# Performance work log

Hardware: AMD Instinct MI355X
Metric: run time of the kernel (lower is better)

## Reference

```python
import jax, jax.numpy as jnp
import numpy as np

N, M, D = 4, 512, 1024
H = 16
DK = D // H


def setup_inputs() -> dict:
    rng = jax.random.key(0)
    ks = jax.random.split(rng, 11)
    w = lambda k: jax.random.normal(k, (D, D), jnp.float32) * 0.02
    b = lambda k: jax.random.normal(k, (D,), jnp.float32) * 0.02
    return {
        "query": jax.random.normal(ks[0], (N, M, D), jnp.float32),
        "key": jax.random.normal(ks[1], (N, M, D), jnp.float32),
        "value": jax.random.normal(ks[2], (N, M, D), jnp.float32),
        "Wq": w(ks[3]), "bq": b(ks[4]),
        "Wk": w(ks[5]), "bk": b(ks[6]),
        "Wv": w(ks[7]), "bv": b(ks[8]),
        "Wo": w(ks[9]), "bo": b(ks[10]),
    }


def reference(query, key, value, Wq, bq, Wk, bk, Wv, bv, Wo, bo):
    n, m, d = query.shape
    h, dk = H, d // H
    # torch Linear: y = x @ W.T + b
    q = (query @ Wq.T + bq).reshape(n, m, h, dk)
    k = (key @ Wk.T + bk).reshape(n, m, h, dk)
    v = (value @ Wv.T + bv).reshape(n, m, h, dk)
    # per-token channel outer product: [n,m,h,dk,dk]
    scores = jnp.einsum('nmhd,nmhq->nmhdq', q, k) / np.float32(np.sqrt(dk))
    p_attn = jax.nn.softmax(scores, axis=-1)
    # contract score block with value channels: [n,m,h,dk]
    ctx = jnp.einsum('nmhdq,nmhq->nmhd', p_attn, v).reshape(n, m, d)
    return ctx @ Wo.T + bo
```

## Files before the change

### kernel.cpp

```cpp
#include <hip/hip_runtime.h>
#include <hip/hip_bf16.h>
#include <stdint.h>
#include <stddef.h>

typedef __bf16 bf16_t;
typedef __attribute__((ext_vector_type(8))) __bf16 bf16x8;
typedef __attribute__((ext_vector_type(4))) float f32x4;
typedef __attribute__((ext_vector_type(2))) float f32x2;

#define TOK 2048
#define DMODEL 1024
#define NHEAD 16

__device__ __forceinline__ void gload_lds16(const void* g, void* l) {
  __builtin_amdgcn_global_load_lds(
      (const __attribute__((address_space(1))) void*)g,
      (__attribute__((address_space(3))) void*)l, 16, 0, 0);
}

struct CvtArgs {
  const float* src[7];
  bf16_t* dst[7];
  int n[7];
};

__global__ __launch_bounds__(256) void cvt_kernel(CvtArgs a) {
  const int arr = blockIdx.y;
  const int n = a.n[arr];
  const int i = blockIdx.x;
  int base;
  if (arr < 3) {
    const int xcd = i & 7, s = i >> 3;
    base = xcd * (256 * DMODEL) + s * 2048;
  } else {
    base = i * 2048;
  }
  const int e = base + threadIdx.x * 8;
  if (e >= n) return;
  const float* s = a.src[arr];
  bf16_t* d = a.dst[arr];
  f32x4 x0 = *(const f32x4*)(s + e);
  f32x4 x1 = *(const f32x4*)(s + e + 4);
  bf16x8 o;
  o[0] = (bf16_t)x0[0]; o[1] = (bf16_t)x0[1]; o[2] = (bf16_t)x0[2]; o[3] = (bf16_t)x0[3];
  o[4] = (bf16_t)x1[0]; o[5] = (bf16_t)x1[1]; o[6] = (bf16_t)x1[2]; o[7] = (bf16_t)x1[3];
  *(bf16x8*)(d + e) = o;
}

struct GArgs {
  const bf16_t* A[3];
  const bf16_t* W[3];
  const float* bias[3];
  void* C[3];
};

template <bool QKV3, int MI, int NJ, int OCC, typename CT>
__global__ __launch_bounds__(256, OCC) void gemmS(GArgs g) {
  constexpr int K = DMODEL, N = DMODEL;
  constexpr int nt = K / 64;
  constexpr int AR = 32 * MI;
  constexpr int BR = 32 * NJ;

  const int i = blockIdx.x;
  const int xcd = i & 7, slot = i >> 3;
  int z, bm, bn;
  if (QKV3) {
    z = slot >> 5;
    const int s = slot & 31;
    bm = (xcd * 2 + (s >> 4)) * AR;
    bn = (s & 15) * BR;
  } else {
    z = 0;
    bm = (xcd * 4 + (slot >> 5)) * AR;
    bn = (slot & 31) * BR;
  }

  const bf16_t* __restrict__ A = g.A[z];
  const bf16_t* __restrict__ W = g.W[z];
  const float* __restrict__ bias = g.bias[z];
  CT* __restrict__ C = (CT*)g.C[z];

  __shared__ alignas(16) bf16_t As[2][AR * 64];
  __shared__ alignas(16) bf16_t Bs[2][BR * 64];

  const int tid = threadIdx.x;
  const int wv = tid >> 6, lane = tid & 63;
  const int wr = (wv >> 1) * (16 * MI);
  const int wc = (wv & 1) * (16 * NJ);
  const int lm = lane & 15, lch = lane >> 4;
  const int cr4 = (lane >> 4) * 4;

  const int sr8 = lane >> 3;
  const int sc = (lane & 7) ^ sr8;
  const bf16_t* Asrc = A + (size_t)(bm + wv * 8 * MI + sr8) * K + sc * 8;
  const bf16_t* Wsrc = W + (size_t)(bn + wv * 8 * NJ + sr8) * K + sc * 8;

  f32x4 acc[MI][NJ] = {};

#define STAGE(T)                                                               \
  {                                                                            \
    const int _b = (T) & 1;                                                    \
    _Pragma("unroll") for (int j = 0; j < MI; ++j)                             \
        gload_lds16(Asrc + (size_t)(j * 8) * K + (T) * 64,                     \
                    &As[_b][(wv * 8 * MI + j * 8) * 64]);                      \
    _Pragma("unroll") for (int j = 0; j < NJ; ++j)                             \
        gload_lds16(Wsrc + (size_t)(j * 8) * K + (T) * 64,                     \
                    &Bs[_b][(wv * 8 * NJ + j * 8) * 64]);                      \
  }

  STAGE(0);

#pragma unroll 1
  for (int T = 0; T < nt; ++T) {
    __syncthreads();
    if (T + 1 < nt) STAGE(T + 1);
    __builtin_amdgcn_sched_barrier(0);

    const int b = T & 1;
#pragma unroll
    for (int kk = 0; kk < 2; ++kk) {
      bf16x8 fa[MI], fb[NJ];
#pragma unroll
      for (int ii = 0; ii < MI; ++ii) {
        const int ra = wr + ii * 16 + lm;
        fa[ii] = *(const bf16x8*)&As[b][ra * 64 + (((kk * 4 + lch) ^ (ra & 7)) * 8)];
      }
#pragma unroll
      for (int jj = 0; jj < NJ; ++jj) {
        const int rb = wc + jj * 16 + lm;
        fb[jj] = *(const bf16x8*)&Bs[b][rb * 64 + (((kk * 4 + lch) ^ (rb & 7)) * 8)];
      }
#pragma unroll
      for (int ii = 0; ii < MI; ++ii)
#pragma unroll
        for (int jj = 0; jj < NJ; ++jj)
          acc[ii][jj] = __builtin_amdgcn_mfma_f32_16x16x32_bf16(
              fa[ii], fb[jj], acc[ii][jj], 0, 0, 0);
    }
  }
#undef STAGE

#pragma unroll
  for (int ii = 0; ii < MI; ++ii)
#pragma unroll
    for (int jj = 0; jj < NJ; ++jj) {
      const int col = bn + wc + jj * 16 + lm;
      const float bvv = bias[col];
#pragma unroll
      for (int r = 0; r < 4; ++r) {
        const int row = bm + wr + ii * 16 + cr4 + r;
        C[(size_t)row * N + col] = (CT)(acc[ii][jj][r] + bvv);
      }
    }
}

__global__ __launch_bounds__(256) void attn_kernel(
    const bf16_t* __restrict__ q, const bf16_t* __restrict__ k,
    const bf16_t* __restrict__ v, bf16_t* __restrict__ ctx) {
  __shared__ float kS[4][64];
  __shared__ float vS[4][64];
  const int wv = threadIdx.x >> 6, lane = threadIdx.x & 63;
  const int i = blockIdx.x;
  const int xcd = i & 7, j = i >> 3;
  const int p = j * 4 + wv;
  const int pair = (xcd * 256 + (p >> 4)) * NHEAD + (p & 15);
  const size_t base = (size_t)pair * 64;
  const float sc = 0.125f * 1.44269504088896341f;
  const float qd = (float)q[base + lane];
  kS[wv][lane] = (float)k[base + lane];
  vS[wv][lane] = (float)v[base + lane];
  asm volatile("s_waitcnt lgkmcnt(0)" ::: "memory");
  const float a = qd * sc;
  const f32x2 av = {a, a};
  f32x2 sum = {0.f, 0.f}, acc = {0.f, 0.f};
#pragma unroll
  for (int jj = 0; jj < 64; jj += 4) {
    f32x4 k4 = *(const f32x4*)&kS[wv][jj];
    f32x4 v4 = *(const f32x4*)&vS[wv][jj];
    f32x2 t0 = av * (f32x2){k4[0], k4[1]};
    f32x2 t1 = av * (f32x2){k4[2], k4[3]};
    f32x2 e0 = {__builtin_amdgcn_exp2f(t0[0]), __builtin_amdgcn_exp2f(t0[1])};
    f32x2 e1 = {__builtin_amdgcn_exp2f(t1[0]), __builtin_amdgcn_exp2f(t1[1])};
    sum += e0 + e1;
    acc += e0 * (f32x2){v4[0], v4[1]} + e1 * (f32x2){v4[2], v4[3]};
  }
  const float s = sum[0] + sum[1];
  const float o = acc[0] + acc[1];
  ctx[base + lane] = (bf16_t)(o * __builtin_amdgcn_rcpf(s));
}

extern "C" void kernel_launch(void* const* d_in, const int* in_sizes, int n_in,
                              void* d_out, int out_size, void* d_ws, size_t ws_size,
                              hipStream_t stream) {
  const float* query = (const float*)d_in[0];
  const float* key   = (const float*)d_in[1];
  const float* value = (const float*)d_in[2];
  const float* Wq = (const float*)d_in[3];
  const float* bq = (const float*)d_in[4];
  const float* Wk = (const float*)d_in[5];
  const float* bk = (const float*)d_in[6];
  const float* Wv = (const float*)d_in[7];
  const float* bv = (const float*)d_in[8];
  const float* Wo = (const float*)d_in[9];
  const float* bo = (const float*)d_in[10];
  float* out = (float*)d_out;

  const size_t XE = (size_t)TOK * DMODEL;
  const size_t WE = (size_t)DMODEL * DMODEL;

  char* ws = (char*)d_ws;
  size_t off = 0;
  bf16_t* xb[3];
  for (int i = 0; i < 3; ++i) { xb[i] = (bf16_t*)(ws + off); off += XE * 2; }
  bf16_t* wb[4];
  for (int i = 0; i < 4; ++i) { wb[i] = (bf16_t*)(ws + off); off += WE * 2; }
  bf16_t* pb[3];
  for (int i = 0; i < 3; ++i) { pb[i] = (bf16_t*)(ws + off); off += XE * 2; }
  bf16_t* ctxb = (bf16_t*)(ws + off); off += XE * 2;

  CvtArgs ca;
  ca.src[0] = query; ca.src[1] = key; ca.src[2] = value;
  ca.src[3] = Wq; ca.src[4] = Wk; ca.src[5] = Wv; ca.src[6] = Wo;
  ca.dst[0] = xb[0]; ca.dst[1] = xb[1]; ca.dst[2] = xb[2];
  ca.dst[3] = wb[0]; ca.dst[4] = wb[1]; ca.dst[5] = wb[2]; ca.dst[6] = wb[3];
  ca.n[0] = ca.n[1] = ca.n[2] = (int)XE;
  ca.n[3] = ca.n[4] = ca.n[5] = ca.n[6] = (int)WE;
  cvt_kernel<<<dim3((unsigned)(XE / (256 * 8)), 7), 256, 0, stream>>>(ca);

  GArgs g1;
  g1.A[0] = xb[0]; g1.A[1] = xb[1]; g1.A[2] = xb[2];
  g1.W[0] = wb[0]; g1.W[1] = wb[1]; g1.W[2] = wb[2];
  g1.bias[0] = bq; g1.bias[1] = bk; g1.bias[2] = bv;
  g1.C[0] = pb[0]; g1.C[1] = pb[1]; g1.C[2] = pb[2];
  gemmS<true, 4, 2, 3, bf16_t><<<dim3(768), 256, 0, stream>>>(g1);

  attn_kernel<<<dim3(TOK * NHEAD / 4), 256, 0, stream>>>(pb[0], pb[1], pb[2], ctxb);

  GArgs g2;
  g2.A[0] = ctxb; g2.W[0] = wb[3]; g2.bias[0] = bo; g2.C[0] = out;
  g2.A[1] = ctxb; g2.W[1] = wb[3]; g2.bias[1] = bo; g2.C[1] = out;
  g2.A[2] = ctxb; g2.W[2] = wb[3]; g2.bias[2] = bo; g2.C[2] = out;
  gemmS<false, 2, 1, 3, float><<<dim3(1024), 256, 0, stream>>>(g2);
}
```

Measured before the change: 62.00 us.

## Add triple-buffered K=32 QKV GEMM with explicit vmcnt waits

Replaces the fused QKV projection GEMM with a dedicated kernel that loads K-tiles of 32 instead of 64 into a three-deep LDS ring buffer. Each iteration waits with a partial vmcnt and keeps two tiles in flight, rather than double-buffering behind a full __syncthreads. A new XOR swizzle is matched to the 32-wide rows. The aim is to hide global-to-LDS latency better; the cost is twice as many iterations and barriers, and it depends on the vmcnt counts being correct.

```diff
diff --git a/kernel.cpp b/kernel.cpp
--- a/kernel.cpp
+++ b/kernel.cpp
@@ -54,7 +54,107 @@
   void* C[3];
 };
 
-template <bool QKV3, int MI, int NJ, int OCC, typename CT>
+__global__ __launch_bounds__(256, 3) void gemmQ(GArgs g) {
+  constexpr int K = DMODEL, N = DMODEL;
+  constexpr int nt = K / 32;
+  constexpr int MI = 4, NJ = 2;
+
+  const int i = blockIdx.x;
+  const int xcd = i & 7, slot = i >> 3;
+  const int z = slot >> 5;
+  const int s = slot & 31;
+  const int bm = (xcd * 2 + (s >> 4)) * 128;
+  const int bn = (s & 15) * 64;
+
+  const bf16_t* __restrict__ A = g.A[z];
+  const bf16_t* __restrict__ W = g.W[z];
+  const float* __restrict__ bias = g.bias[z];
+  bf16_t* __restrict__ C = (bf16_t*)g.C[z];
+
+  __shared__ alignas(16) bf16_t As[3][128 * 32];
+  __shared__ alignas(16) bf16_t Bs[3][64 * 32];
+
+  const int tid = threadIdx.x;
+  const int wv = tid >> 6, lane = tid & 63;
+  const int wr = (wv >> 1) * 64;
+  const int wc = (wv & 1) * 32;
+  const int lm = lane & 15, lch = lane >> 4;
+  const int cr4 = (lane >> 4) * 4;
+
+  const int rg = lane >> 2, ch = lane & 3;
+#define XR(r) ((((r) & 3) + (((r) >> 2) & 3)) & 3)
+  const int ra0 = wv * 32 + rg, ra1 = wv * 32 + 16 + rg;
+  const bf16_t* Asrc0 = A + (size_t)(bm + ra0) * K + (ch ^ XR(ra0)) * 8;
+  const bf16_t* Asrc1 = A + (size_t)(bm + ra1) * K + (ch ^ XR(ra1)) * 8;
+  const int rb0 = wv * 16 + rg;
+  const bf16_t* Wsrc0 = W + (size_t)(bn + rb0) * K + (ch ^ XR(rb0)) * 8;
+
+  f32x4 acc[MI][NJ] = {};
+
+#define STAGE(T, B_)                                                           \
+  {                                                                            \
+    gload_lds16(Asrc0 + (T) * 32, &As[B_][(wv * 32) * 32]);                    \
+    gload_lds16(Asrc1 + (T) * 32, &As[B_][(wv * 32 + 16) * 32]);               \
+    gload_lds16(Wsrc0 + (T) * 32, &Bs[B_][(wv * 16) * 32]);                    \
+  }
+
+  STAGE(0, 0);
+  STAGE(1, 1);
+
+  int bT = 0, bS = 2;
+#pragma unroll 1
+  for (int T = 0; T < nt; ++T) {
+    if (T + 1 < nt) {
+      asm volatile("s_waitcnt vmcnt(3)" ::: "memory");
+    } else {
+      asm volatile("s_waitcnt vmcnt(0)" ::: "memory");
+    }
+    __builtin_amdgcn_sched_barrier(0);
+    __builtin_amdgcn_s_barrier();
+    __builtin_amdgcn_sched_barrier(0);
+
+    if (T + 2 < nt) STAGE(T + 2, bS);
+    __builtin_amdgcn_sched_barrier(0);
+
+    bf16x8 fa[MI], fb[NJ];
+#pragma unroll
+    for (int ii = 0; ii < MI; ++ii) {
+      const int r = wr + ii * 16 + lm;
+      fa[ii] = *(const bf16x8*)&As[bT][r * 32 + ((lch ^ XR(r)) * 8)];
+    }
+#pragma unroll
+    for (int jj = 0; jj < NJ; ++jj) {
+      const int r = wc + jj * 16 + lm;
+      fb[jj] = *(const bf16x8*)&Bs[bT][r * 32 + ((lch ^ XR(r)) * 8)];
+    }
+#pragma unroll
+    for (int ii = 0; ii < MI; ++ii)
+#pragma unroll
+      for (int jj = 0; jj < NJ; ++jj)
+        acc[ii][jj] = __builtin_amdgcn_mfma_f32_16x16x32_bf16(
+            fa[ii], fb[jj], acc[ii][jj], 0, 0, 0);
+
+    bT = (bT == 2) ? 0 : bT + 1;
+    bS = (bS == 2) ? 0 : bS + 1;
+  }
+#undef STAGE
+#undef XR
+
+#pragma unroll
+  for (int ii = 0; ii < MI; ++ii)
+#pragma unroll
+    for (int jj = 0; jj < NJ; ++jj) {
+      const int col = bn + wc + jj * 16 + lm;
+      const float bvv = bias[col];
+#pragma unroll
+      for (int r = 0; r < 4; ++r) {
+        const int row = bm + wr + ii * 16 + cr4 + r;
+        C[(size_t)row * N + col] = (bf16_t)(acc[ii][jj][r] + bvv);
+      }
+    }
+}
+
+template <int MI, int NJ, int OCC, typename CT>
 __global__ __launch_bounds__(256, OCC) void gemmS(GArgs g) {
   constexpr int K = DMODEL, N = DMODEL;
   constexpr int nt = K / 64;
@@ -63,17 +163,9 @@
 
   const int i = blockIdx.x;
   const int xcd = i & 7, slot = i >> 3;
-  int z, bm, bn;
-  if (QKV3) {
-    z = slot >> 5;
-    const int s = slot & 31;
-    bm = (xcd * 2 + (s >> 4)) * AR;
-    bn = (s & 15) * BR;
-  } else {
-    z = 0;
-    bm = (xcd * 4 + (slot >> 5)) * AR;
-    bn = (slot & 31) * BR;
-  }
+  const int z = 0;
+  const int bm = (xcd * 4 + (slot >> 5)) * AR;
+  const int bn = (slot & 31) * BR;
 
   const bf16_t* __restrict__ A = g.A[z];
   const bf16_t* __restrict__ W = g.W[z];
@@ -232,7 +324,7 @@
   g1.W[0] = wb[0]; g1.W[1] = wb[1]; g1.W[2] = wb[2];
   g1.bias[0] = bq; g1.bias[1] = bk; g1.bias[2] = bv;
   g1.C[0] = pb[0]; g1.C[1] = pb[1]; g1.C[2] = pb[2];
-  gemmS<true, 4, 2, 3, bf16_t><<<dim3(768), 256, 0, stream>>>(g1);
+  gemmQ<<<dim3(768), 256, 0, stream>>>(g1);
 
   attn_kernel<<<dim3(TOK * NHEAD / 4), 256, 0, stream>>>(pb[0], pb[1], pb[2], ctxb);
 
@@ -240,5 +332,5 @@
   g2.A[0] = ctxb; g2.W[0] = wb[3]; g2.bias[0] = bo; g2.C[0] = out;
   g2.A[1] = ctxb; g2.W[1] = wb[3]; g2.bias[1] = bo; g2.C[1] = out;
   g2.A[2] = ctxb; g2.W[2] = wb[3]; g2.bias[2] = bo; g2.C[2] = out;
-  gemmS<false, 2, 1, 3, float><<<dim3(1024), 256, 0, stream>>>(g2);
-}
+  gemmS<2, 1, 3, float><<<dim3(1024), 256, 0, stream>>>(g2);
+}
```

After: 68.94 us. 1.11x slower.
